# Kernel optimization log

Hardware: AMD Instinct MI355X
Metric: run time of the kernel (lower is better)

The kernel has to match this reference:

```python
import jax, jax.numpy as jnp
import numpy as np

SEQ, B, N = 128, 64, 128
IN_DIM, HID = 64, 128
K = 2          # max_diffusion_step
L = 2          # num_rnn_layers
M = K + 1      # num_matrices = n_supports*K + 1 (one 'laplacian' support)


def setup_inputs() -> dict:
    key = jax.random.key(0)
    ks = jax.random.split(key, 8)
    inputs = jax.random.normal(ks[0], (SEQ, B, N, IN_DIM), jnp.float32)
    initial_hidden_state = jnp.zeros((L, B, N * HID), jnp.float32)
    # scaled normalized-laplacian-like support; 1/N keeps chebyshev terms bounded
    supports = jax.random.normal(ks[1], (1, N, N), jnp.float32) / N

    def w(k, fan_in, out):
        return jax.random.normal(k, (fan_in, out), jnp.float32) / np.sqrt(fan_in).astype(np.float32)

    in0 = M * (IN_DIM + HID)   # layer 0 gconv input features (576)
    in1 = M * (HID + HID)      # layer 1 gconv input features (768)
    return {
        "inputs": inputs,
        "initial_hidden_state": initial_hidden_state,
        "supports": supports,
        "Wg0": w(ks[2], in0, 2 * HID), "bg0": jnp.zeros((2 * HID,), jnp.float32),
        "Wc0": w(ks[3], in0, HID),     "bc0": jnp.zeros((HID,), jnp.float32),
        "Wg1": w(ks[4], in1, 2 * HID), "bg1": jnp.zeros((2 * HID,), jnp.float32),
        "Wc1": w(ks[5], in1, HID),     "bc1": jnp.zeros((HID,), jnp.float32),
    }


def _gconv(x, support, W, b):
    # x: (B, N, F). Chebyshev diffusion: x0, x1=S@x0, x_k=2*S@x_{k-1}-x_{k-2}
    x0 = x
    x1 = jnp.einsum('mn,bnf->bmf', support, x0)
    mats = [x0, x1]
    for _ in range(2, K + 1):
        x2 = 2.0 * jnp.einsum('mn,bnf->bmf', support, x1) - x0
        mats.append(x2)
        x0, x1 = x1, x2
    xs = jnp.stack(mats, axis=-1)                 # (B, N, F, M) -- torch layout
    xs = xs.reshape(x.shape[0], x.shape[1], -1)   # (B, N, F*M)
    return xs @ W + b                             # (B, N, out)


def _dcgru_layer(x_seq, h0, support, Wg, bg, Wc, bc):
    # x_seq: (T, B, N, F); h0: (B, N, HID)
    def step(h, x_t):
        cat = jnp.concatenate([x_t, h], axis=-1)
        gates = jax.nn.sigmoid(_gconv(cat, support, Wg, bg))
        r, u = jnp.split(gates, 2, axis=-1)
        c = jnp.tanh(_gconv(jnp.concatenate([x_t, r * h], axis=-1), support, Wc, bc))
        h_new = u * h + (1.0 - u) * c
        return h_new, h_new
    return jax.lax.scan(step, h0, x_seq)


def reference(inputs, initial_hidden_state, supports, Wg0, bg0, Wc0, bc0, Wg1, bg1, Wc1, bc1):
    sup = supports[0]
    h0_0 = initial_hidden_state[0].reshape(B, N, HID)
    h0_1 = initial_hidden_state[1].reshape(B, N, HID)
    h_last0, ys0 = _dcgru_layer(inputs, h0_0, sup, Wg0, bg0, Wc0, bc0)
    h_last1, ys1 = _dcgru_layer(ys0, h0_1, sup, Wg1, bg1, Wc1, bc1)
    output_hidden = jnp.stack([h_last0, h_last1], axis=0).reshape(L, B, N * HID)
    outputs = ys1.reshape(SEQ, B, N * HID)
    return output_hidden, outputs
```

## Files before the change

### kernel.cpp

```cpp
#include <hip/hip_runtime.h>
#include <math.h>

#define SEQ 128
#define B 64
#define NN 128
#define IN_DIM 64
#define HID 128
#define BNH (B*NN*HID)

typedef unsigned short u16;
typedef __bf16 bf16x8 __attribute__((ext_vector_type(8)));
typedef float f32x4 __attribute__((ext_vector_type(4)));

__device__ __forceinline__ u16 f2bf(float f) {
    union { float f; unsigned u; } x; x.f = f;
    unsigned r = x.u + 0x7fffu + ((x.u >> 16) & 1u);
    return (u16)(r >> 16);
}
__device__ __forceinline__ float bf2f(u16 b) {
    union { unsigned u; float f; } x; x.u = ((unsigned)b) << 16; return x.f;
}
__device__ __forceinline__ bf16x8 ld_frag(const u16* p) {
    union { uint4 q; bf16x8 v; } u;
    u.q = *(const uint4*)p;
    return u.v;
}
__device__ __forceinline__ uint2 pack4(const f32x4& a) {
    uint2 pk;
    pk.x = (unsigned)f2bf(a[0]) | ((unsigned)f2bf(a[1]) << 16);
    pk.y = (unsigned)f2bf(a[2]) | ((unsigned)f2bf(a[3]) << 16);
    return pk;
}
__device__ __forceinline__ bf16x8 cvt8(const float* p) {
    float4 v0 = *(const float4*)p, v1 = *(const float4*)(p + 4);
    union { uint4 q; bf16x8 v; } t;
    t.q.x = (unsigned)f2bf(v0.x) | ((unsigned)f2bf(v0.y) << 16);
    t.q.y = (unsigned)f2bf(v0.z) | ((unsigned)f2bf(v0.w) << 16);
    t.q.z = (unsigned)f2bf(v1.x) | ((unsigned)f2bf(v1.y) << 16);
    t.q.w = (unsigned)f2bf(v1.z) | ((unsigned)f2bf(v1.w) << 16);
    return t.v;
}

__global__ void prep_A2_kernel(const float* __restrict__ S, u16* __restrict__ A2bf) {
    int idx = blockIdx.x * 256 + threadIdx.x;
    int m = idx >> 7, n = idx & 127;
    A2bf[idx] = f2bf(S[idx]);
    float acc = 0.f;
    #pragma unroll 4
    for (int k = 0; k < 128; ++k) acc += S[m*128 + k] * S[k*128 + n];
    A2bf[16384 + idx] = f2bf(2.f*acc - (m == n ? 1.f : 0.f));
}

__global__ void prep_A2f_kernel(const u16* __restrict__ A2bf, u16* __restrict__ A2f) {
    int idx = blockIdx.x * 256 + threadIdx.x;
    int j = idx & 7, lane = (idx >> 3) & 63, g = (idx >> 9) & 15, kc = idx >> 13;
    int mp = g*16 + (lane & 15);
    int n  = kc*32 + (lane >> 4)*8 + j;
    A2f[idx] = A2bf[mp*128 + n];
}

__global__ void prep_WTf_kernel(const float* __restrict__ W, u16* __restrict__ WTf,
                                int F, int NO) {
    int KK = 3 * F;
    int idx = blockIdx.x * 256 + threadIdx.x;
    if (idx >= NO * KK) return;
    int per = 512 * (NO/16);
    int kc = idx / per, rem = idx % per;
    int cg = rem >> 9, lane = (rem >> 3) & 63, j = idx & 7;
    int col = cg*16 + (lane & 15);
    int k = kc*32 + (lane >> 4)*8 + j;
    int m = k / F, f = k - m*F;
    WTf[idx] = f2bf(W[(size_t)(f*3 + m) * NO + col]);
}

__global__ void cast2_kernel(const float* __restrict__ in, u16* __restrict__ o0,
                             u16* __restrict__ o1) {
    int i = blockIdx.x * 256 + threadIdx.x;
    if (i < BNH) o0[i] = f2bf(in[i]);
    else o1[i - BNH] = f2bf(in[i]);
}

template<int L>
__device__ __forceinline__ void bodyA(
    int b, int nh,
    const float* __restrict__ xf, const u16* __restrict__ xb,
    const u16* __restrict__ hb, const u16* __restrict__ A2f,
    const u16* __restrict__ WTf, const float* __restrict__ bias,
    u16* __restrict__ rh, float* __restrict__ ubuf, u16* __restrict__ xsgF,
    u16* smem)
{
    constexpr int FIN = L ? 128 : 64;
    constexpr int F   = L ? 256 : 192;
    constexpr int KK  = 3 * F;
    const int tid = threadIdx.x;
    const int lane = tid & 63, w = tid >> 6;
    const int l15 = lane & 15, l16 = lane >> 4;

    for (int task = tid; task < 128 * (F/8); task += 512) {
        int n = task & 127, f8 = (task >> 7) * 8;
        int bn = b*NN + n;
        union { uint4 q; u16 s[8]; } t;
        if (f8 < FIN) {
            if (L == 0) { union { uint4 q; bf16x8 v; } c; c.v = cvt8(xf + (size_t)bn*IN_DIM + f8); t.q = c.q; }
            else t.q = *(const uint4*)(xb + (size_t)bn*HID + f8);
        } else t.q = *(const uint4*)(hb + (size_t)bn*HID + (f8 - FIN));
        #pragma unroll
        for (int i = 0; i < 8; ++i)
            smem[(f8+i)*128 + (n ^ (((f8+i) & 7)*8))] = t.s[i];
    }
    __syncthreads();

    constexpr int NFW = F / 32;
    const int mg2 = w & 3, fg2 = w >> 2;
    const int f0w = fg2 * (F/2);
    f32x4 dacc[NFW][4];
    #pragma unroll
    for (int ff = 0; ff < NFW; ++ff)
        #pragma unroll
        for (int mm = 0; mm < 4; ++mm) dacc[ff][mm] = (f32x4)(0.f);

    #pragma unroll
    for (int kc = 0; kc < 4; ++kc) {
        bf16x8 bfr[4];
        #pragma unroll
        for (int mm = 0; mm < 4; ++mm)
            bfr[mm] = ld_frag(A2f + ((kc*16 + mg2*4 + mm)*64 + lane)*8);
        #pragma unroll
        for (int ff = 0; ff < NFW; ++ff) {
            const int f = f0w + ff*16 + l15;
            bf16x8 afr = ld_frag(&smem[f*128 + ((kc*32 + l16*8) ^ ((f & 7)*8))]);
            #pragma unroll
            for (int mm = 0; mm < 4; ++mm)
                dacc[ff][mm] = __builtin_amdgcn_mfma_f32_16x16x32_bf16(afr, bfr[mm], dacc[ff][mm], 0, 0, 0);
        }
    }
    __syncthreads();

    #pragma unroll
    for (int ff = 0; ff < NFW; ++ff) {
        const int f4 = f0w + ff*16 + l16*4;
        #pragma unroll
        for (int mm = 0; mm < 4; ++mm) {
            const int mp = mg2*64 + mm*16 + l15;
            uint2 pk = pack4(dacc[ff][mm]);
            *(uint2*)&smem[mp*F + (f4 ^ ((mp & 7)*8))] = pk;
            if (f4 < FIN) {
                const int slot = mp >> 7, node = mp & 127;
                size_t off = ((((size_t)b*2 + slot)*(FIN/32) + (f4 >> 5))*8 + (node >> 4))*512
                           + (((f4 >> 3) & 3)*16 + (node & 15))*8 + (f4 & 7);
                *(uint2*)(xsgF + off) = pk;
            }
        }
    }
    __syncthreads();

    const int mg = w & 1, ng = w >> 1;
    f32x4 pacc[4][2];
    #pragma unroll
    for (int fi = 0; fi < 4; ++fi)
        #pragma unroll
        for (int gj = 0; gj < 2; ++gj) pacc[fi][gj] = (f32x4)(0.f);

    #pragma unroll
    for (int kc = 0; kc < KK/32; ++kc) {
        const int k = kc*32, m = k / F, fIn = k - m*F;
        bf16x8 bb[2];
        #pragma unroll
        for (int gj = 0; gj < 2; ++gj)
            bb[gj] = ld_frag(WTf + (((size_t)kc*16 + nh*8 + ng*2 + gj)*64 + lane)*8);
        #pragma unroll
        for (int fi = 0; fi < 4; ++fi) {
            const int node = mg*64 + fi*16 + l15;
            bf16x8 a;
            if (m == 0) {
                const int bn = b*NN + node, f = fIn + l16*8;
                if (f < FIN) {
                    if (L == 0) a = cvt8(xf + (size_t)bn*IN_DIM + f);
                    else        a = ld_frag(xb + (size_t)bn*HID + f);
                } else a = ld_frag(hb + (size_t)bn*HID + (f - FIN));
            } else {
                const int mp = (m-1)*128 + node;
                a = ld_frag(&smem[mp*F + ((fIn + l16*8) ^ ((mp & 7)*8))]);
            }
            #pragma unroll
            for (int gj = 0; gj < 2; ++gj)
                pacc[fi][gj] = __builtin_amdgcn_mfma_f32_16x16x32_bf16(a, bb[gj], pacc[fi][gj], 0, 0, 0);
        }
    }
    #pragma unroll
    for (int fi = 0; fi < 4; ++fi) {
        #pragma unroll
        for (int gj = 0; gj < 2; ++gj) {
            const int colL = ng*32 + gj*16 + l15;
            const float bc = bias[nh*128 + colL];
            #pragma unroll
            for (int r = 0; r < 4; ++r) {
                const int node = mg*64 + fi*16 + l16*4 + r;
                const int bn = b*NN + node;
                const float v = pacc[fi][gj][r] + bc;
                const float s = 1.f / (1.f + expf(-v));
                if (nh == 0) {
                    float h = bf2f(hb[(size_t)bn*HID + colL]);
                    rh[(size_t)bn*HID + colL] = f2bf(s * h);
                } else {
                    ubuf[(size_t)bn*HID + colL] = s;
                }
            }
        }
    }
}

template<int L>
__device__ __forceinline__ void bodyB(
    int b, int nh,
    const float* __restrict__ xf, const u16* __restrict__ xb,
    const u16* __restrict__ rh, const float* __restrict__ ubuf,
    const u16* __restrict__ xsgF, const u16* __restrict__ A2f,
    const u16* __restrict__ WTf, const float* __restrict__ bias,
    const float* __restrict__ hfR, float* __restrict__ hfW,
    u16* __restrict__ hbfW, float* __restrict__ out2,
    u16* smem)
{
    constexpr int FIN = L ? 128 : 64;
    constexpr int F   = L ? 256 : 192;
    constexpr int KK  = 3 * F;
    constexpr int CW  = FIN + 128;
    u16* rhT  = smem;
    u16* catN = smem + 128*128;
    u16* xsL2 = catN + 64*CW;
    const int tid = threadIdx.x;
    const int lane = tid & 63, w = tid >> 6;
    const int l15 = lane & 15, l16 = lane >> 4;

    for (int task = tid; task < 128*16; task += 512) {
        int n = task & 127, f8 = (task >> 7) * 8;
        union { uint4 q; u16 s[8]; } t;
        t.q = *(const uint4*)(rh + (size_t)(b*NN + n)*HID + f8);
        #pragma unroll
        for (int i = 0; i < 8; ++i)
            rhT[(f8+i)*128 + (n ^ (((f8+i) & 7)*8))] = t.s[i];
    }
    for (int task = tid; task < 64*(CW/8); task += 512) {
        int nl = task & 63, f8 = (task >> 6) * 8;
        int bn = b*NN + nh*64 + nl;
        uint4 q;
        if (f8 < FIN) {
            if (L == 0) { union { uint4 q; bf16x8 v; } c; c.v = cvt8(xf + (size_t)bn*IN_DIM + f8); q = c.q; }
            else q = *(const uint4*)(xb + (size_t)bn*HID + f8);
        } else q = *(const uint4*)(rh + (size_t)bn*HID + (f8 - FIN));
        *(uint4*)&catN[nl*CW + (f8 ^ ((nl & 7)*8))] = q;
    }
    __syncthreads();

    const int mgB = w & 3, fgB = w >> 2;
    const int f0w = fgB*64, ml0 = mgB*32;
    f32x4 dacc[4][2];
    #pragma unroll
    for (int ff = 0; ff < 4; ++ff)
        #pragma unroll
        for (int mm = 0; mm < 2; ++mm) dacc[ff][mm] = (f32x4)(0.f);

    #pragma unroll
    for (int kc = 0; kc < 4; ++kc) {
        bf16x8 bfr[2];
        #pragma unroll
        for (int mm = 0; mm < 2; ++mm) {
            const int mlb = ml0 + mm*16;
            const int g = (mlb >> 6)*8 + nh*4 + ((mlb & 63) >> 4);
            bfr[mm] = ld_frag(A2f + ((kc*16 + g)*64 + lane)*8);
        }
        #pragma unroll
        for (int ff = 0; ff < 4; ++ff) {
            const int f = f0w + ff*16 + l15;
            bf16x8 afr = ld_frag(&rhT[f*128 + ((kc*32 + l16*8) ^ ((f & 7)*8))]);
            #pragma unroll
            for (int mm = 0; mm < 2; ++mm)
                dacc[ff][mm] = __builtin_amdgcn_mfma_f32_16x16x32_bf16(afr, bfr[mm], dacc[ff][mm], 0, 0, 0);
        }
    }
    #pragma unroll
    for (int ff = 0; ff < 4; ++ff) {
        const int f4 = f0w + ff*16 + l16*4;
        #pragma unroll
        for (int mm = 0; mm < 2; ++mm) {
            const int ml = ml0 + mm*16 + l15;
            *(uint2*)&xsL2[ml*128 + (f4 ^ ((ml & 7)*8))] = pack4(dacc[ff][mm]);
        }
    }
    __syncthreads();

    const int mg = w & 1, ng = w >> 1;
    f32x4 cacc[2][2];
    #pragma unroll
    for (int fi = 0; fi < 2; ++fi)
        #pragma unroll
        for (int gj = 0; gj < 2; ++gj) cacc[fi][gj] = (f32x4)(0.f);

    #pragma unroll
    for (int kc = 0; kc < KK/32; ++kc) {
        const int k = kc*32, m = k / F, fIn = k - m*F;
        bf16x8 bb[2];
        #pragma unroll
        for (int gj = 0; gj < 2; ++gj)
            bb[gj] = ld_frag(WTf + (((size_t)kc*8 + ng*2 + gj)*64 + lane)*8);
        #pragma unroll
        for (int fi = 0; fi < 2; ++fi) {
            const int nl = mg*32 + fi*16 + l15;
            bf16x8 a;
            if (m == 0) {
                a = ld_frag(&catN[nl*CW + ((fIn + l16*8) ^ ((nl & 7)*8))]);
            } else if (fIn < FIN) {
                size_t off = ((((size_t)b*2 + (m-1))*(FIN/32) + (fIn >> 5))*8 + (nh*4 + mg*2 + fi))*512
                           + (size_t)lane*8;
                a = ld_frag(xsgF + off);
            } else {
                const int ml = (m-1)*64 + nl;
                a = ld_frag(&xsL2[ml*128 + (((fIn - FIN) + l16*8) ^ ((ml & 7)*8))]);
            }
            #pragma unroll
            for (int gj = 0; gj < 2; ++gj)
                cacc[fi][gj] = __builtin_amdgcn_mfma_f32_16x16x32_bf16(a, bb[gj], cacc[fi][gj], 0, 0, 0);
        }
    }
    #pragma unroll
    for (int fi = 0; fi < 2; ++fi) {
        #pragma unroll
        for (int gj = 0; gj < 2; ++gj) {
            const int col = ng*32 + gj*16 + l15;
            const float bc = bias[col];
            #pragma unroll
            for (int r = 0; r < 4; ++r) {
                const int node = nh*64 + mg*32 + fi*16 + l16*4 + r;
                const int bn = b*NN + node;
                const float v = cacc[fi][gj][r] + bc;
                const float c = tanhf(v);
                const float u = ubuf[(size_t)bn*HID + col];
                const float ho = hfR[(size_t)bn*HID + col];
                const float hn = u*ho + (1.f - u)*c;
                hfW[(size_t)bn*HID + col] = hn;
                hbfW[(size_t)bn*HID + col] = f2bf(hn);
                if (L == 1) out2[(size_t)bn*HID + col] = hn;
            }
        }
    }
}

__global__ __launch_bounds__(512, 2) void kA(int zoff,
    const float* xf0, const u16* h0r, const u16* h1b, const u16* A2f,
    const u16* WTgf0, const float* bg0, u16* rh0, float* u0, u16* xsgF0,
    const u16* WTgf1, const float* bg1, u16* rh1, float* u1, u16* xsgF1)
{
    extern __shared__ u16 smem[];
    const int b = blockIdx.x, nh = blockIdx.y;
    if ((int)blockIdx.z + zoff == 0)
        bodyA<0>(b, nh, xf0, nullptr, h0r, A2f, WTgf0, bg0, rh0, u0, xsgF0, smem);
    else
        bodyA<1>(b, nh, nullptr, h0r, h1b, A2f, WTgf1, bg1, rh1, u1, xsgF1, smem);
}

__global__ __launch_bounds__(512, 2) void kB(int zoff,
    const float* xf0, const u16* h0r, const u16* A2f,
    const u16* rh0, const float* u0, const u16* xsgF0, const u16* WTcf0, const float* bc0,
    const float* hf0r, float* hf0w, u16* hbf0w,
    const u16* rh1, const float* u1, const u16* xsgF1, const u16* WTcf1, const float* bc1,
    float* hf1, u16* hbf1, float* out2)
{
    extern __shared__ u16 smem[];
    const int b = blockIdx.x, nh = blockIdx.y;
    if ((int)blockIdx.z + zoff == 0)
        bodyB<0>(b, nh, xf0, nullptr, rh0, u0, xsgF0, A2f, WTcf0, bc0, hf0r, hf0w, hbf0w, nullptr, smem);
    else
        bodyB<1>(b, nh, nullptr, h0r, rh1, u1, xsgF1, A2f, WTcf1, bc1, hf1, hf1, hbf1, out2, smem);
}

extern "C" void kernel_launch(void* const* d_in, const int* in_sizes, int n_in,
                              void* d_out, int out_size, void* d_ws, size_t ws_size,
                              hipStream_t stream) {
    (void)in_sizes; (void)n_in; (void)out_size; (void)ws_size;
    const float* inputs = (const float*)d_in[0];
    const float* h_init = (const float*)d_in[1];
    const float* S      = (const float*)d_in[2];
    const float* Wg0 = (const float*)d_in[3];
    const float* bg0 = (const float*)d_in[4];
    const float* Wc0 = (const float*)d_in[5];
    const float* bc0 = (const float*)d_in[6];
    const float* Wg1 = (const float*)d_in[7];
    const float* bg1 = (const float*)d_in[8];
    const float* Wc1 = (const float*)d_in[9];
    const float* bc1 = (const float*)d_in[10];

    float* out = (float*)d_out;
    float* outputs = out + 2 * (size_t)BNH;

    char* ws = (char*)d_ws;
    u16* A2bf  = (u16*)ws;                      ws += 32768 * 2;
    u16* A2f   = (u16*)ws;                      ws += 32768 * 2;
    u16* WTgf0 = (u16*)ws;                      ws += 256*576 * 2;
    u16* WTcf0 = (u16*)ws;                      ws += 128*576 * 2;
    u16* WTgf1 = (u16*)ws;                      ws += 256*768 * 2;
    u16* WTcf1 = (u16*)ws;                      ws += 128*768 * 2;
    ws = (char*)(((size_t)ws + 255) & ~(size_t)255);
    u16* xsgF0 = (u16*)ws;                      ws += (size_t)64*2*2*4096 * 2;
    u16* xsgF1 = (u16*)ws;                      ws += (size_t)64*2*4*4096 * 2;
    u16* rh0 = (u16*)ws;                        ws += (size_t)BNH * 2;
    u16* rh1 = (u16*)ws;                        ws += (size_t)BNH * 2;
    float* u0 = (float*)ws;                     ws += (size_t)BNH * 4;
    float* u1 = (float*)ws;                     ws += (size_t)BNH * 4;
    float* hf0_[2];
    hf0_[0] = (float*)ws;                       ws += (size_t)BNH * 4;
    hf0_[1] = (float*)ws;                       ws += (size_t)BNH * 4;
    float* hf1 = (float*)ws;                    ws += (size_t)BNH * 4;
    u16* hbf0_[2];
    hbf0_[0] = (u16*)ws;                        ws += (size_t)BNH * 2;
    hbf0_[1] = (u16*)ws;                        ws += (size_t)BNH * 2;
    u16* hbf1 = (u16*)ws;                       ws += (size_t)BNH * 2;

    hipFuncSetAttribute((const void*)kA, hipFuncAttributeMaxDynamicSharedMemorySize, 131072);
    hipFuncSetAttribute((const void*)kB, hipFuncAttributeMaxDynamicSharedMemorySize, 98304);

    hipMemcpyAsync(hf0_[1], h_init, (size_t)BNH * sizeof(float), hipMemcpyDeviceToDevice, stream);
    hipMemcpyAsync(hf1, h_init + BNH, (size_t)BNH * sizeof(float), hipMemcpyDeviceToDevice, stream);
    cast2_kernel<<<(2*BNH + 255)/256, 256, 0, stream>>>(h_init, hbf0_[1], hbf1);
    prep_A2_kernel<<<64, 256, 0, stream>>>(S, A2bf);
    prep_A2f_kernel<<<128, 256, 0, stream>>>(A2bf, A2f);
    prep_WTf_kernel<<<(256*576 + 255)/256, 256, 0, stream>>>(Wg0, WTgf0, 192, 256);
    prep_WTf_kernel<<<(128*576 + 255)/256, 256, 0, stream>>>(Wc0, WTcf0, 192, 128);
    prep_WTf_kernel<<<(256*768 + 255)/256, 256, 0, stream>>>(Wg1, WTgf1, 256, 256);
    prep_WTf_kernel<<<(128*768 + 255)/256, 256, 0, stream>>>(Wc1, WTcf1, 256, 128);

    for (int tau = 0; tau <= SEQ; ++tau) {
        const int nz = (tau == 0 || tau == SEQ) ? 1 : 2;
        const int zoff = (tau == SEQ) ? 1 : 0;
        const int rb = (tau + 1) & 1, wb = tau & 1;
        const int tx = (tau < SEQ) ? tau : (SEQ - 1);
        const float* xt = inputs + (size_t)tx * B * NN * IN_DIM;
        const u16* h0r = hbf0_[rb];
        float* out2 = outputs + (size_t)((tau > 0) ? tau - 1 : 0) * BNH;

        kA<<<dim3(64, 2, nz), 512, 131072, stream>>>(zoff,
            xt, h0r, hbf1, A2f,
            WTgf0, bg0, rh0, u0, xsgF0,
            WTgf1, bg1, rh1, u1, xsgF1);
        kB<<<dim3(64, 2, nz), 512, 98304, stream>>>(zoff,
            xt, h0r, A2f,
            rh0, u0, xsgF0, WTcf0, bc0, hf0_[rb], hf0_[wb], hbf0_[wb],
            rh1, u1, xsgF1, WTcf1, bc1, hf1, hbf1, out2);
    }
    hipMemcpyAsync(out, hf0_[1], (size_t)BNH * sizeof(float), hipMemcpyDeviceToDevice, stream);
    hipMemcpyAsync(out + BNH, hf1, (size_t)BNH * sizeof(float), hipMemcpyDeviceToDevice, stream);
}
```

Baseline: 8.466 ms.

## Fuse gate and candidate gconv into one per-step kernel with transposed hidden state

The separate gate (kA) and candidate (kB) kernels are merged into one kStep kernel per timestep. Each block now computes the full reset gate for all nodes of its batch, so the r*h diffusion for the candidate is done locally in shared memory. This removes the xsgF spill buffer, the second launch, and the global round trip between the two stages. Hidden state is also kept in a transposed bf16 copy so shared-memory staging uses vector loads instead of scalar transposes. The cost is redundant reset-gate work in both column-half blocks, an extra transposed write per step, and double-buffered layer-1 state.

```diff
diff --git a/kernel.cpp b/kernel.cpp
--- a/kernel.cpp
+++ b/kernel.cpp
@@ -73,20 +73,33 @@
     WTf[idx] = f2bf(W[(size_t)(f*3 + m) * NO + col]);
 }
 
-__global__ void cast2_kernel(const float* __restrict__ in, u16* __restrict__ o0,
-                             u16* __restrict__ o1) {
+__global__ void init_h_kernel(const float* __restrict__ h,
+                              u16* __restrict__ hbf0, u16* __restrict__ h0T,
+                              u16* __restrict__ hbf1, u16* __restrict__ h1T) {
     int i = blockIdx.x * 256 + threadIdx.x;
-    if (i < BNH) o0[i] = f2bf(in[i]);
-    else o1[i - BNH] = f2bf(in[i]);
+    int which = (i >= BNH);
+    int j = which ? i - BNH : i;
+    u16 v = f2bf(h[i]);
+    int bn = j >> 7, col = j & 127;
+    if (!which) { hbf0[j] = v; h0T[(size_t)col*8192 + bn] = v; }
+    else        { hbf1[j] = v; h1T[(size_t)col*8192 + bn] = v; }
 }
 
 template<int L>
-__device__ __forceinline__ void bodyA(
+__device__ __forceinline__ void step_body(
     int b, int nh,
-    const float* __restrict__ xf, const u16* __restrict__ xb,
-    const u16* __restrict__ hb, const u16* __restrict__ A2f,
-    const u16* __restrict__ WTf, const float* __restrict__ bias,
-    u16* __restrict__ rh, float* __restrict__ ubuf, u16* __restrict__ xsgF,
+    const float* __restrict__ xf,
+    const u16* __restrict__ hbX,
+    const u16* __restrict__ xT,
+    const u16* __restrict__ hbH,
+    const u16* __restrict__ hTH,
+    const u16* __restrict__ A2f,
+    const u16* __restrict__ WTg, const float* __restrict__ bg,
+    const u16* __restrict__ WTc, const float* __restrict__ bc,
+    u16* __restrict__ rhb, float* __restrict__ ub,
+    const float* __restrict__ hfR, float* __restrict__ hfW,
+    u16* __restrict__ hbfW, u16* __restrict__ hTW,
+    float* __restrict__ out2,
     u16* smem)
 {
     constexpr int FIN = L ? 128 : 64;
@@ -96,281 +109,258 @@
     const int lane = tid & 63, w = tid >> 6;
     const int l15 = lane & 15, l16 = lane >> 4;
 
-    for (int task = tid; task < 128 * (F/8); task += 512) {
-        int n = task & 127, f8 = (task >> 7) * 8;
-        int bn = b*NN + n;
-        union { uint4 q; u16 s[8]; } t;
-        if (f8 < FIN) {
-            if (L == 0) { union { uint4 q; bf16x8 v; } c; c.v = cvt8(xf + (size_t)bn*IN_DIM + f8); t.q = c.q; }
-            else t.q = *(const uint4*)(xb + (size_t)bn*HID + f8);
-        } else t.q = *(const uint4*)(hb + (size_t)bn*HID + (f8 - FIN));
-        #pragma unroll
-        for (int i = 0; i < 8; ++i)
-            smem[(f8+i)*128 + (n ^ (((f8+i) & 7)*8))] = t.s[i];
+    if (L == 0) {
+        for (int task = tid; task < 1024; task += 512) {
+            int ng8 = task & 15, f = task >> 4, n0 = ng8*8, bn = b*NN + n0;
+            union { uint4 q; u16 s[8]; } t;
+            #pragma unroll
+            for (int i = 0; i < 8; ++i) t.s[i] = f2bf(xf[(size_t)(bn + i)*IN_DIM + f]);
+            *(uint4*)&smem[f*128 + (n0 ^ ((f & 7)*8))] = t.q;
+        }
+    }
+    {
+        const int R0 = L ? 0 : 64;
+        const int NT = (F - R0) * 16;
+        for (int task = tid; task < NT; task += 512) {
+            int ng8 = task & 15, f = R0 + (task >> 4);
+            const u16* src;
+            if (L == 1) src = (f < 128) ? (xT + (size_t)f*8192) : (hTH + (size_t)(f - 128)*8192);
+            else        src = hTH + (size_t)(f - 64)*8192;
+            uint4 q = *(const uint4*)(src + (size_t)b*128 + ng8*8);
+            *(uint4*)&smem[f*128 + ((ng8*8) ^ ((f & 7)*8))] = q;
+        }
     }
     __syncthreads();
 
-    constexpr int NFW = F / 32;
-    const int mg2 = w & 3, fg2 = w >> 2;
-    const int f0w = fg2 * (F/2);
-    f32x4 dacc[NFW][4];
+    {
+        constexpr int NFW = F / 32;
+        const int mg2 = w & 3, f0w = (w >> 2) * (F/2);
+        f32x4 dacc[NFW][4];
+        #pragma unroll
+        for (int ff = 0; ff < NFW; ++ff)
+            #pragma unroll
+            for (int mm = 0; mm < 4; ++mm) dacc[ff][mm] = (f32x4)(0.f);
+        #pragma unroll
+        for (int kc = 0; kc < 4; ++kc) {
+            bf16x8 bfr[4];
+            #pragma unroll
+            for (int mm = 0; mm < 4; ++mm)
+                bfr[mm] = ld_frag(A2f + (((size_t)kc*16 + mg2*4 + mm)*64 + lane)*8);
+            #pragma unroll
+            for (int ff = 0; ff < NFW; ++ff) {
+                const int fr = f0w + ff*16 + l15;
+                bf16x8 afr = ld_frag(&smem[fr*128 + ((kc*32 + l16*8) ^ ((fr & 7)*8))]);
+                #pragma unroll
+                for (int mm = 0; mm < 4; ++mm)
+                    dacc[ff][mm] = __builtin_amdgcn_mfma_f32_16x16x32_bf16(afr, bfr[mm], dacc[ff][mm], 0, 0, 0);
+            }
+        }
+        __syncthreads();
+        #pragma unroll
+        for (int ff = 0; ff < NFW; ++ff) {
+            const int f4 = f0w + ff*16 + l16*4;
+            #pragma unroll
+            for (int mm = 0; mm < 4; ++mm) {
+                const int mp = mg2*64 + mm*16 + l15;
+                *(uint2*)&smem[mp*F + (f4 ^ ((mp & 7)*8))] = pack4(dacc[ff][mm]);
+            }
+        }
+    }
+    __syncthreads();
+
+    const int mg = w & 1, ng = w >> 1;
+    {
+        f32x4 pacc[4][3];
+        #pragma unroll
+        for (int fi = 0; fi < 4; ++fi)
+            #pragma unroll
+            for (int gj = 0; gj < 3; ++gj) pacc[fi][gj] = (f32x4)(0.f);
+
+        #pragma unroll
+        for (int kc = 0; kc < KK/32; ++kc) {
+            const int k = kc*32, m = k / F, fl = k - m*F;
+            bf16x8 bb[3];
+            #pragma unroll
+            for (int gj = 0; gj < 3; ++gj) {
+                const int c0 = ng*48 + gj*16;
+                const int ca = (c0 < 128) ? c0 : 128 + nh*64 + (c0 - 128);
+                bb[gj] = ld_frag(WTg + (((size_t)kc*16 + (ca >> 4))*64 + lane)*8);
+            }
+            #pragma unroll
+            for (int fi = 0; fi < 4; ++fi) {
+                const int node = mg*64 + fi*16 + l15;
+                bf16x8 a;
+                if (m == 0) {
+                    const int bn = b*NN + node;
+                    if (fl < FIN) {
+                        if (L == 0) a = cvt8(xf + (size_t)bn*IN_DIM + fl + l16*8);
+                        else        a = ld_frag(hbX + (size_t)bn*HID + fl + l16*8);
+                    } else a = ld_frag(hbH + (size_t)bn*HID + (fl - FIN) + l16*8);
+                } else {
+                    const int mp = (m - 1)*128 + node;
+                    a = ld_frag(&smem[mp*F + ((fl + l16*8) ^ ((mp & 7)*8))]);
+                }
+                #pragma unroll
+                for (int gj = 0; gj < 3; ++gj)
+                    pacc[fi][gj] = __builtin_amdgcn_mfma_f32_16x16x32_bf16(a, bb[gj], pacc[fi][gj], 0, 0, 0);
+            }
+        }
+        __syncthreads();
+
+        #pragma unroll
+        for (int fi = 0; fi < 4; ++fi) {
+            const int node0 = mg*64 + fi*16 + l16*4;
+            #pragma unroll
+            for (int gj = 0; gj < 3; ++gj) {
+                const int c0 = ng*48 + gj*16;
+                if (c0 < 128) {
+                    const int c = c0 + l15;
+                    union { uint2 q; u16 s[4]; } pk;
+                    #pragma unroll
+                    for (int r = 0; r < 4; ++r) {
+                        const int bn = b*NN + node0 + r;
+                        const float v = pacc[fi][gj][r] + bg[c];
+                        const float s = 1.f/(1.f + expf(-v));
+                        const u16 rv = f2bf(s * bf2f(hbH[(size_t)bn*HID + c]));
+                        pk.s[r] = rv;
+                        rhb[(size_t)bn*HID + c] = rv;
+                    }
+                    *(uint2*)&smem[c*F + FIN + (node0 ^ ((c & 7)*8))] = pk.q;
+                } else {
+                    const int uc = nh*64 + (c0 - 128) + l15;
+                    const float bcv = bg[128 + uc];
+                    #pragma unroll
+                    for (int r = 0; r < 4; ++r) {
+                        const int bn = b*NN + node0 + r;
+                        const float v = pacc[fi][gj][r] + bcv;
+                        ub[(size_t)bn*HID + uc] = 1.f/(1.f + expf(-v));
+                    }
+                }
+            }
+        }
+    }
+    __syncthreads();
+
+    const int cmg = w & 1, cng = w >> 1;
+    f32x4 cacc[4];
     #pragma unroll
-    for (int ff = 0; ff < NFW; ++ff)
-        #pragma unroll
-        for (int mm = 0; mm < 4; ++mm) dacc[ff][mm] = (f32x4)(0.f);
+    for (int fi = 0; fi < 4; ++fi) cacc[fi] = (f32x4)(0.f);
 
     #pragma unroll
-    for (int kc = 0; kc < 4; ++kc) {
-        bf16x8 bfr[4];
-        #pragma unroll
-        for (int mm = 0; mm < 4; ++mm)
-            bfr[mm] = ld_frag(A2f + ((kc*16 + mg2*4 + mm)*64 + lane)*8);
-        #pragma unroll
-        for (int ff = 0; ff < NFW; ++ff) {
-            const int f = f0w + ff*16 + l15;
-            bf16x8 afr = ld_frag(&smem[f*128 + ((kc*32 + l16*8) ^ ((f & 7)*8))]);
-            #pragma unroll
-            for (int mm = 0; mm < 4; ++mm)
-                dacc[ff][mm] = __builtin_amdgcn_mfma_f32_16x16x32_bf16(afr, bfr[mm], dacc[ff][mm], 0, 0, 0);
-        }
-    }
-    __syncthreads();
+    for (int kc = 0; kc < F/32; ++kc) {
+        const int fl = kc*32;
+        bf16x8 bb = ld_frag(WTc + (((size_t)kc*8 + nh*4 + cng)*64 + lane)*8);
+        #pragma unroll
+        for (int fi = 0; fi < 4; ++fi) {
+            const int node = cmg*64 + fi*16 + l15;
+            const int bn = b*NN + node;
+            bf16x8 a;
+            if (fl < FIN) {
+                if (L == 0) a = cvt8(xf + (size_t)bn*IN_DIM + fl + l16*8);
+                else        a = ld_frag(hbX + (size_t)bn*HID + fl + l16*8);
+            } else a = ld_frag(rhb + (size_t)bn*HID + (fl - FIN) + l16*8);
+            cacc[fi] = __builtin_amdgcn_mfma_f32_16x16x32_bf16(a, bb, cacc[fi], 0, 0, 0);
+        }
+    }
 
     #pragma unroll
-    for (int ff = 0; ff < NFW; ++ff) {
-        const int f4 = f0w + ff*16 + l16*4;
-        #pragma unroll
-        for (int mm = 0; mm < 4; ++mm) {
-            const int mp = mg2*64 + mm*16 + l15;
-            uint2 pk = pack4(dacc[ff][mm]);
-            *(uint2*)&smem[mp*F + (f4 ^ ((mp & 7)*8))] = pk;
-            if (f4 < FIN) {
-                const int slot = mp >> 7, node = mp & 127;
-                size_t off = ((((size_t)b*2 + slot)*(FIN/32) + (f4 >> 5))*8 + (node >> 4))*512
-                           + (((f4 >> 3) & 3)*16 + (node & 15))*8 + (f4 & 7);
-                *(uint2*)(xsgF + off) = pk;
-            }
-        }
-    }
-    __syncthreads();
-
-    const int mg = w & 1, ng = w >> 1;
-    f32x4 pacc[4][2];
-    #pragma unroll
-    for (int fi = 0; fi < 4; ++fi)
-        #pragma unroll
-        for (int gj = 0; gj < 2; ++gj) pacc[fi][gj] = (f32x4)(0.f);
-
-    #pragma unroll
-    for (int kc = 0; kc < KK/32; ++kc) {
-        const int k = kc*32, m = k / F, fIn = k - m*F;
-        bf16x8 bb[2];
-        #pragma unroll
-        for (int gj = 0; gj < 2; ++gj)
-            bb[gj] = ld_frag(WTf + (((size_t)kc*16 + nh*8 + ng*2 + gj)*64 + lane)*8);
-        #pragma unroll
-        for (int fi = 0; fi < 4; ++fi) {
-            const int node = mg*64 + fi*16 + l15;
-            bf16x8 a;
-            if (m == 0) {
-                const int bn = b*NN + node, f = fIn + l16*8;
-                if (f < FIN) {
-                    if (L == 0) a = cvt8(xf + (size_t)bn*IN_DIM + f);
-                    else        a = ld_frag(xb + (size_t)bn*HID + f);
-                } else a = ld_frag(hb + (size_t)bn*HID + (f - FIN));
-            } else {
-                const int mp = (m-1)*128 + node;
-                a = ld_frag(&smem[mp*F + ((fIn + l16*8) ^ ((mp & 7)*8))]);
-            }
-            #pragma unroll
-            for (int gj = 0; gj < 2; ++gj)
-                pacc[fi][gj] = __builtin_amdgcn_mfma_f32_16x16x32_bf16(a, bb[gj], pacc[fi][gj], 0, 0, 0);
-        }
-    }
+    for (int slot = 0; slot < 2; ++slot) {
+        f32x4 d2[4][2];
+        #pragma unroll
+        for (int ff = 0; ff < 4; ++ff)
+            #pragma unroll
+            for (int mm = 0; mm < 2; ++mm) d2[ff][mm] = (f32x4)(0.f);
+        const int sf0 = (w & 1)*64, sn0 = (w >> 1)*32;
+        #pragma unroll
+        for (int kc = 0; kc < 4; ++kc) {
+            bf16x8 bfr[2];
+            #pragma unroll
+            for (int mm = 0; mm < 2; ++mm) {
+                const int g = slot*8 + ((sn0 + mm*16) >> 4);
+                bfr[mm] = ld_frag(A2f + (((size_t)kc*16 + g)*64 + lane)*8);
+            }
+            #pragma unroll
+            for (int ff = 0; ff < 4; ++ff) {
+                const int c = sf0 + ff*16 + l15;
+                bf16x8 afr = ld_frag(&smem[c*F + FIN + ((kc*32 + l16*8) ^ ((c & 7)*8))]);
+                #pragma unroll
+                for (int mm = 0; mm < 2; ++mm)
+                    d2[ff][mm] = __builtin_amdgcn_mfma_f32_16x16x32_bf16(afr, bfr[mm], d2[ff][mm], 0, 0, 0);
+            }
+        }
+        __syncthreads();
+        #pragma unroll
+        for (int ff = 0; ff < 4; ++ff) {
+            const int f4 = sf0 + ff*16 + l16*4;
+            #pragma unroll
+            for (int mm = 0; mm < 2; ++mm) {
+                const int node = sn0 + mm*16 + l15;
+                *(uint2*)&smem[(128 + node)*F + FIN + (f4 ^ ((node & 7)*8))] = pack4(d2[ff][mm]);
+            }
+        }
+        __syncthreads();
+        #pragma unroll
+        for (int kc = 0; kc < F/32; ++kc) {
+            const int fl = kc*32;
+            const int kcg = (slot + 1)*(F/32) + kc;
+            bf16x8 bb = ld_frag(WTc + (((size_t)kcg*8 + nh*4 + cng)*64 + lane)*8);
+            #pragma unroll
+            for (int fi = 0; fi < 4; ++fi) {
+                const int node = cmg*64 + fi*16 + l15;
+                bf16x8 a;
+                if (fl < FIN) {
+                    const int mp = slot*128 + node;
+                    a = ld_frag(&smem[mp*F + ((fl + l16*8) ^ ((mp & 7)*8))]);
+                } else {
+                    a = ld_frag(&smem[(128 + node)*F + FIN + (((fl - FIN) + l16*8) ^ ((node & 7)*8))]);
+                }
+                cacc[fi] = __builtin_amdgcn_mfma_f32_16x16x32_bf16(a, bb, cacc[fi], 0, 0, 0);
+            }
+        }
+    }
+
+    const int col = nh*64 + cng*16 + l15;
+    const float bcv = bc[col];
     #pragma unroll
     for (int fi = 0; fi < 4; ++fi) {
-        #pragma unroll
-        for (int gj = 0; gj < 2; ++gj) {
-            const int colL = ng*32 + gj*16 + l15;
-            const float bc = bias[nh*128 + colL];
-            #pragma unroll
-            for (int r = 0; r < 4; ++r) {
-                const int node = mg*64 + fi*16 + l16*4 + r;
-                const int bn = b*NN + node;
-                const float v = pacc[fi][gj][r] + bc;
-                const float s = 1.f / (1.f + expf(-v));
-                if (nh == 0) {
-                    float h = bf2f(hb[(size_t)bn*HID + colL]);
-                    rh[(size_t)bn*HID + colL] = f2bf(s * h);
-                } else {
-                    ubuf[(size_t)bn*HID + colL] = s;
-                }
-            }
-        }
-    }
-}
-
-template<int L>
-__device__ __forceinline__ void bodyB(
-    int b, int nh,
-    const float* __restrict__ xf, const u16* __restrict__ xb,
-    const u16* __restrict__ rh, const float* __restrict__ ubuf,
-    const u16* __restrict__ xsgF, const u16* __restrict__ A2f,
-    const u16* __restrict__ WTf, const float* __restrict__ bias,
-    const float* __restrict__ hfR, float* __restrict__ hfW,
-    u16* __restrict__ hbfW, float* __restrict__ out2,
-    u16* smem)
-{
-    constexpr int FIN = L ? 128 : 64;
-    constexpr int F   = L ? 256 : 192;
-    constexpr int KK  = 3 * F;
-    constexpr int CW  = FIN + 128;
-    u16* rhT  = smem;
-    u16* catN = smem + 128*128;
-    u16* xsL2 = catN + 64*CW;
-    const int tid = threadIdx.x;
-    const int lane = tid & 63, w = tid >> 6;
-    const int l15 = lane & 15, l16 = lane >> 4;
-
-    for (int task = tid; task < 128*16; task += 512) {
-        int n = task & 127, f8 = (task >> 7) * 8;
-        union { uint4 q; u16 s[8]; } t;
-        t.q = *(const uint4*)(rh + (size_t)(b*NN + n)*HID + f8);
-        #pragma unroll
-        for (int i = 0; i < 8; ++i)
-            rhT[(f8+i)*128 + (n ^ (((f8+i) & 7)*8))] = t.s[i];
-    }
-    for (int task = tid; task < 64*(CW/8); task += 512) {
-        int nl = task & 63, f8 = (task >> 6) * 8;
-        int bn = b*NN + nh*64 + nl;
-        uint4 q;
-        if (f8 < FIN) {
-            if (L == 0) { union { uint4 q; bf16x8 v; } c; c.v = cvt8(xf + (size_t)bn*IN_DIM + f8); q = c.q; }
-            else q = *(const uint4*)(xb + (size_t)bn*HID + f8);
-        } else q = *(const uint4*)(rh + (size_t)bn*HID + (f8 - FIN));
-        *(uint4*)&catN[nl*CW + (f8 ^ ((nl & 7)*8))] = q;
-    }
-    __syncthreads();
-
-    const int mgB = w & 3, fgB = w >> 2;
-    const int f0w = fgB*64, ml0 = mgB*32;
-    f32x4 dacc[4][2];
-    #pragma unroll
-    for (int ff = 0; ff < 4; ++ff)
-        #pragma unroll
-        for (int mm = 0; mm < 2; ++mm) dacc[ff][mm] = (f32x4)(0.f);
-
-    #pragma unroll
-    for (int kc = 0; kc < 4; ++kc) {
-        bf16x8 bfr[2];
-        #pragma unroll
-        for (int mm = 0; mm < 2; ++mm) {
-            const int mlb = ml0 + mm*16;
-            const int g = (mlb >> 6)*8 + nh*4 + ((mlb & 63) >> 4);
-            bfr[mm] = ld_frag(A2f + ((kc*16 + g)*64 + lane)*8);
-        }
-        #pragma unroll
-        for (int ff = 0; ff < 4; ++ff) {
-            const int f = f0w + ff*16 + l15;
-            bf16x8 afr = ld_frag(&rhT[f*128 + ((kc*32 + l16*8) ^ ((f & 7)*8))]);
-            #pragma unroll
-            for (int mm = 0; mm < 2; ++mm)
-                dacc[ff][mm] = __builtin_amdgcn_mfma_f32_16x16x32_bf16(afr, bfr[mm], dacc[ff][mm], 0, 0, 0);
-        }
-    }
-    #pragma unroll
-    for (int ff = 0; ff < 4; ++ff) {
-        const int f4 = f0w + ff*16 + l16*4;
-        #pragma unroll
-        for (int mm = 0; mm < 2; ++mm) {
-            const int ml = ml0 + mm*16 + l15;
-            *(uint2*)&xsL2[ml*128 + (f4 ^ ((ml & 7)*8))] = pack4(dacc[ff][mm]);
-        }
-    }
-    __syncthreads();
-
-    const int mg = w & 1, ng = w >> 1;
-    f32x4 cacc[2][2];
-    #pragma unroll
-    for (int fi = 0; fi < 2; ++fi)
-        #pragma unroll
-        for (int gj = 0; gj < 2; ++gj) cacc[fi][gj] = (f32x4)(0.f);
-
-    #pragma unroll
-    for (int kc = 0; kc < KK/32; ++kc) {
-        const int k = kc*32, m = k / F, fIn = k - m*F;
-        bf16x8 bb[2];
-        #pragma unroll
-        for (int gj = 0; gj < 2; ++gj)
-            bb[gj] = ld_frag(WTf + (((size_t)kc*8 + ng*2 + gj)*64 + lane)*8);
-        #pragma unroll
-        for (int fi = 0; fi < 2; ++fi) {
-            const int nl = mg*32 + fi*16 + l15;
-            bf16x8 a;
-            if (m == 0) {
-                a = ld_frag(&catN[nl*CW + ((fIn + l16*8) ^ ((nl & 7)*8))]);
-            } else if (fIn < FIN) {
-                size_t off = ((((size_t)b*2 + (m-1))*(FIN/32) + (fIn >> 5))*8 + (nh*4 + mg*2 + fi))*512
-                           + (size_t)lane*8;
-                a = ld_frag(xsgF + off);
-            } else {
-                const int ml = (m-1)*64 + nl;
-                a = ld_frag(&xsL2[ml*128 + (((fIn - FIN) + l16*8) ^ ((ml & 7)*8))]);
-            }
-            #pragma unroll
-            for (int gj = 0; gj < 2; ++gj)
-                cacc[fi][gj] = __builtin_amdgcn_mfma_f32_16x16x32_bf16(a, bb[gj], cacc[fi][gj], 0, 0, 0);
-        }
-    }
-    #pragma unroll
-    for (int fi = 0; fi < 2; ++fi) {
-        #pragma unroll
-        for (int gj = 0; gj < 2; ++gj) {
-            const int col = ng*32 + gj*16 + l15;
-            const float bc = bias[col];
-            #pragma unroll
-            for (int r = 0; r < 4; ++r) {
-                const int node = nh*64 + mg*32 + fi*16 + l16*4 + r;
-                const int bn = b*NN + node;
-                const float v = cacc[fi][gj][r] + bc;
-                const float c = tanhf(v);
-                const float u = ubuf[(size_t)bn*HID + col];
-                const float ho = hfR[(size_t)bn*HID + col];
-                const float hn = u*ho + (1.f - u)*c;
-                hfW[(size_t)bn*HID + col] = hn;
-                hbfW[(size_t)bn*HID + col] = f2bf(hn);
-                if (L == 1) out2[(size_t)bn*HID + col] = hn;
-            }
-        }
-    }
-}
-
-__global__ __launch_bounds__(512, 2) void kA(int zoff,
-    const float* xf0, const u16* h0r, const u16* h1b, const u16* A2f,
-    const u16* WTgf0, const float* bg0, u16* rh0, float* u0, u16* xsgF0,
-    const u16* WTgf1, const float* bg1, u16* rh1, float* u1, u16* xsgF1)
+        const int node0 = cmg*64 + fi*16 + l16*4;
+        union { uint2 q; u16 s[4]; } pk;
+        #pragma unroll
+        for (int r = 0; r < 4; ++r) {
+            const int bn = b*NN + node0 + r;
+            const float v = cacc[fi][r] + bcv;
+            const float cnd = tanhf(v);
+            const float uu = ub[(size_t)bn*HID + col];
+            const float ho = hfR[(size_t)bn*HID + col];
+            const float hn = uu*ho + (1.f - uu)*cnd;
+            hfW[(size_t)bn*HID + col] = hn;
+            const u16 hv = f2bf(hn);
+            hbfW[(size_t)bn*HID + col] = hv;
+            pk.s[r] = hv;
+            if (L == 1) out2[(size_t)bn*HID + col] = hn;
+        }
+        *(uint2*)&hTW[(size_t)col*8192 + (size_t)b*128 + node0] = pk.q;
+    }
+}
+
+__global__ __launch_bounds__(512, 2) void kStep(int zoff,
+    const float* xf, const u16* A2f,
+    const u16* hbf0r, const u16* h0Tr, const float* hf0r, float* hf0w, u16* hbf0w, u16* h0Tw,
+    const u16* WTgf0, const float* bg0, const u16* WTcf0, const float* bc0, u16* rhb0, float* ub0,
+    const u16* hbf1r, const u16* h1Tr, const float* hf1r, float* hf1w, u16* hbf1w, u16* h1Tw,
+    const u16* WTgf1, const float* bg1, const u16* WTcf1, const float* bc1, u16* rhb1, float* ub1,
+    float* out2)
 {
     extern __shared__ u16 smem[];
     const int b = blockIdx.x, nh = blockIdx.y;
     if ((int)blockIdx.z + zoff == 0)
-        bodyA<0>(b, nh, xf0, nullptr, h0r, A2f, WTgf0, bg0, rh0, u0, xsgF0, smem);
+        step_body<0>(b, nh, xf, nullptr, nullptr, hbf0r, h0Tr, A2f,
+                     WTgf0, bg0, WTcf0, bc0, rhb0, ub0,
+                     hf0r, hf0w, hbf0w, h0Tw, nullptr, smem);
     else
-        bodyA<1>(b, nh, nullptr, h0r, h1b, A2f, WTgf1, bg1, rh1, u1, xsgF1, smem);
-}
-
-__global__ __launch_bounds__(512, 2) void kB(int zoff,
-    const float* xf0, const u16* h0r, const u16* A2f,
-    const u16* rh0, const float* u0, const u16* xsgF0, const u16* WTcf0, const float* bc0,
-    const float* hf0r, float* hf0w, u16* hbf0w,
-    const u16* rh1, const float* u1, const u16* xsgF1, const u16* WTcf1, const float* bc1,
-    float* hf1, u16* hbf1, float* out2)
-{
-    extern __shared__ u16 smem[];
-    const int b = blockIdx.x, nh = blockIdx.y;
-    if ((int)blockIdx.z + zoff == 0)
-        bodyB<0>(b, nh, xf0, nullptr, rh0, u0, xsgF0, A2f, WTcf0, bc0, hf0r, hf0w, hbf0w, nullptr, smem);
-    else
-        bodyB<1>(b, nh, nullptr, h0r, rh1, u1, xsgF1, A2f, WTcf1, bc1, hf1, hf1, hbf1, out2, smem);
+        step_body<1>(b, nh, nullptr, hbf0r, h0Tr, hbf1r, h1Tr, A2f,
+                     WTgf1, bg1, WTcf1, bc1, rhb1, ub1,
+                     hf1r, hf1w, hbf1w, h1Tw, out2, smem);
 }
 
 extern "C" void kernel_launch(void* const* d_in, const int* in_sizes, int n_in,
@@ -400,27 +390,26 @@
     u16* WTgf1 = (u16*)ws;                      ws += 256*768 * 2;
     u16* WTcf1 = (u16*)ws;                      ws += 128*768 * 2;
     ws = (char*)(((size_t)ws + 255) & ~(size_t)255);
-    u16* xsgF0 = (u16*)ws;                      ws += (size_t)64*2*2*4096 * 2;
-    u16* xsgF1 = (u16*)ws;                      ws += (size_t)64*2*4*4096 * 2;
-    u16* rh0 = (u16*)ws;                        ws += (size_t)BNH * 2;
-    u16* rh1 = (u16*)ws;                        ws += (size_t)BNH * 2;
-    float* u0 = (float*)ws;                     ws += (size_t)BNH * 4;
-    float* u1 = (float*)ws;                     ws += (size_t)BNH * 4;
-    float* hf0_[2];
-    hf0_[0] = (float*)ws;                       ws += (size_t)BNH * 4;
-    hf0_[1] = (float*)ws;                       ws += (size_t)BNH * 4;
-    float* hf1 = (float*)ws;                    ws += (size_t)BNH * 4;
-    u16* hbf0_[2];
-    hbf0_[0] = (u16*)ws;                        ws += (size_t)BNH * 2;
-    hbf0_[1] = (u16*)ws;                        ws += (size_t)BNH * 2;
-    u16* hbf1 = (u16*)ws;                       ws += (size_t)BNH * 2;
-
-    hipFuncSetAttribute((const void*)kA, hipFuncAttributeMaxDynamicSharedMemorySize, 131072);
-    hipFuncSetAttribute((const void*)kB, hipFuncAttributeMaxDynamicSharedMemorySize, 98304);
+    u16* rhb0 = (u16*)ws;                       ws += (size_t)BNH * 2;
+    u16* rhb1 = (u16*)ws;                       ws += (size_t)BNH * 2;
+    float* ub0 = (float*)ws;                    ws += (size_t)BNH * 4;
+    float* ub1 = (float*)ws;                    ws += (size_t)BNH * 4;
+    float* hf0_[2]; u16* hbf0_[2]; u16* h0T_[2];
+    float* hf1_[2]; u16* hbf1_[2]; u16* h1T_[2];
+    for (int i = 0; i < 2; ++i) {
+        hf0_[i]  = (float*)ws;                  ws += (size_t)BNH * 4;
+        hf1_[i]  = (float*)ws;                  ws += (size_t)BNH * 4;
+        hbf0_[i] = (u16*)ws;                    ws += (size_t)BNH * 2;
+        hbf1_[i] = (u16*)ws;                    ws += (size_t)BNH * 2;
+        h0T_[i]  = (u16*)ws;                    ws += (size_t)BNH * 2;
+        h1T_[i]  = (u16*)ws;                    ws += (size_t)BNH * 2;
+    }
+
+    hipFuncSetAttribute((const void*)kStep, hipFuncAttributeMaxDynamicSharedMemorySize, 131072);
 
     hipMemcpyAsync(hf0_[1], h_init, (size_t)BNH * sizeof(float), hipMemcpyDeviceToDevice, stream);
-    hipMemcpyAsync(hf1, h_init + BNH, (size_t)BNH * sizeof(float), hipMemcpyDeviceToDevice, stream);
-    cast2_kernel<<<(2*BNH + 255)/256, 256, 0, stream>>>(h_init, hbf0_[1], hbf1);
+    hipMemcpyAsync(hf1_[0], h_init + BNH, (size_t)BNH * sizeof(float), hipMemcpyDeviceToDevice, stream);
+    init_h_kernel<<<(2*BNH + 255)/256, 256, 0, stream>>>(h_init, hbf0_[1], h0T_[1], hbf1_[0], h1T_[0]);
     prep_A2_kernel<<<64, 256, 0, stream>>>(S, A2bf);
     prep_A2f_kernel<<<128, 256, 0, stream>>>(A2bf, A2f);
     prep_WTf_kernel<<<(256*576 + 255)/256, 256, 0, stream>>>(Wg0, WTgf0, 192, 256);
@@ -434,18 +423,16 @@
         const int rb = (tau + 1) & 1, wb = tau & 1;
         const int tx = (tau < SEQ) ? tau : (SEQ - 1);
         const float* xt = inputs + (size_t)tx * B * NN * IN_DIM;
-        const u16* h0r = hbf0_[rb];
         float* out2 = outputs + (size_t)((tau > 0) ? tau - 1 : 0) * BNH;
 
-        kA<<<dim3(64, 2, nz), 512, 131072, stream>>>(zoff,
-            xt, h0r, hbf1, A2f,
-            WTgf0, bg0, rh0, u0, xsgF0,
-            WTgf1, bg1, rh1, u1, xsgF1);
-        kB<<<dim3(64, 2, nz), 512, 98304, stream>>>(zoff,
-            xt, h0r, A2f,
-            rh0, u0, xsgF0, WTcf0, bc0, hf0_[rb], hf0_[wb], hbf0_[wb],
-            rh1, u1, xsgF1, WTcf1, bc1, hf1, hbf1, out2);
+        kStep<<<dim3(64, 2, nz), 512, 131072, stream>>>(zoff,
+            xt, A2f,
+            hbf0_[rb], h0T_[rb], hf0_[rb], hf0_[wb], hbf0_[wb], h0T_[wb],
+            WTgf0, bg0, WTcf0, bc0, rhb0, ub0,
+            hbf1_[rb], h1T_[rb], hf1_[rb], hf1_[wb], hbf1_[wb], h1T_[wb],
+            WTgf1, bg1, WTcf1, bc1, rhb1, ub1,
+            out2);
     }
     hipMemcpyAsync(out, hf0_[1], (size_t)BNH * sizeof(float), hipMemcpyDeviceToDevice, stream);
-    hipMemcpyAsync(out + BNH, hf1, (size_t)BNH * sizeof(float), hipMemcpyDeviceToDevice, stream);
-}
+    hipMemcpyAsync(out + BNH, hf1_[0], (size_t)BNH * sizeof(float), hipMemcpyDeviceToDevice, stream);
+}
```

New measurement: 10.30 ms. 1.22x slower.
